# Performance work log

Measured on AMD Instinct MI355X. Metric: run time of the kernel, lower is better.

## Reference

```python
import jax, jax.numpy as jnp
import numpy as np

B = 32
H = 56
WD = 56
C = 192
NH = 6
WS = 7   # window size
SS = 3   # shift size
HID = 4 * C
N = WS * WS
NW = (H // WS) * (WD // WS)


def _rel_pos_index():
    coords = np.stack(np.meshgrid(np.arange(WS), np.arange(WS), indexing='ij'))  # [2,ws,ws]
    cf = coords.reshape(2, -1)
    rel = cf[:, :, None] - cf[:, None, :]          # [2,N,N]
    rel = rel.transpose(1, 2, 0)
    rel[..., 0] += WS - 1
    rel[..., 1] += WS - 1
    rel[..., 0] *= 2 * WS - 1
    return rel.sum(-1)                              # [N,N] int


def _attn_mask():
    img = np.zeros((H, WD))
    sl = (slice(0, -WS), slice(-WS, -SS), slice(-SS, None))
    cnt = 0
    for hs in sl:
        for ws in sl:
            img[hs, ws] = cnt
            cnt += 1
    mw = img.reshape(H // WS, WS, WD // WS, WS).transpose(0, 2, 1, 3).reshape(-1, N)  # [nW,N]
    d = mw[:, None, :] - mw[:, :, None]
    return np.where(d != 0, -100.0, 0.0).astype(np.float32)  # [nW,N,N]


_RPI = jnp.asarray(_rel_pos_index())
_MASK = jnp.asarray(_attn_mask())


def setup_inputs() -> dict:
    key = jax.random.key(0)
    ks = jax.random.split(key, 8)
    s = 0.02
    return {
        'x': jax.random.normal(ks[0], (B, H * WD, C), jnp.float32),
        'norm1_g': jnp.ones((C,), jnp.float32),
        'norm1_b': jnp.zeros((C,), jnp.float32),
        'qkv_w': jax.random.normal(ks[1], (C, 3 * C), jnp.float32) * s,
        'qkv_b': jnp.zeros((3 * C,), jnp.float32),
        'rel_bias': jax.random.normal(ks[2], ((2 * WS - 1) ** 2, NH), jnp.float32) * s,
        'proj_w': jax.random.normal(ks[3], (C, C), jnp.float32) * s,
        'proj_b': jnp.zeros((C,), jnp.float32),
        'norm2_g': jnp.ones((C,), jnp.float32),
        'norm2_b': jnp.zeros((C,), jnp.float32),
        'fc1_w': jax.random.normal(ks[4], (C, HID), jnp.float32) * s,
        'fc1_b': jnp.zeros((HID,), jnp.float32),
        'fc2_w': jax.random.normal(ks[5], (HID, C), jnp.float32) * s,
        'fc2_b': jnp.zeros((C,), jnp.float32),
    }


def _ln(x, g, b, eps=1e-5):
    m = jnp.mean(x, axis=-1, keepdims=True)
    v = jnp.mean(jnp.square(x - m), axis=-1, keepdims=True)
    return (x - m) / jnp.sqrt(v + eps) * g + b


def reference(x, norm1_g, norm1_b, qkv_w, qkv_b, rel_bias, proj_w, proj_b,
              norm2_g, norm2_b, fc1_w, fc1_b, fc2_w, fc2_b):
    hd = C // NH
    shortcut = x
    xn = _ln(x, norm1_g, norm1_b).reshape(B, H, WD, C)
    xs = jnp.roll(xn, (-SS, -SS), axis=(1, 2))                     # cyclic shift
    # window partition -> [B*nW, N, C]
    xw = xs.reshape(B, H // WS, WS, WD // WS, WS, C)
    xw = xw.transpose(0, 1, 3, 2, 4, 5).reshape(-1, N, C)
    # windowed attention
    qkv = (xw @ qkv_w + qkv_b).reshape(-1, N, 3, NH, hd).transpose(2, 0, 3, 1, 4)
    q, k, v = qkv[0], qkv[1], qkv[2]                               # [B*nW, NH, N, hd]
    attn = jnp.einsum('whnd,whmd->whnm', q * (hd ** -0.5), k)      # [B*nW, NH, N, N]
    bias = rel_bias[_RPI.reshape(-1)].reshape(N, N, NH).transpose(2, 0, 1)
    attn = attn + bias[None]
    attn = attn.reshape(B, NW, NH, N, N) + _MASK[None, :, None]
    attn = jax.nn.softmax(attn.reshape(-1, NH, N, N), axis=-1)
    out = jnp.einsum('whnm,whmd->whnd', attn, v)
    out = out.transpose(0, 2, 1, 3).reshape(-1, N, C)
    out = out @ proj_w + proj_b
    # window reverse + un-shift
    out = out.reshape(B, H // WS, WD // WS, WS, WS, C)
    out = out.transpose(0, 1, 3, 2, 4, 5).reshape(B, H, WD, C)
    out = jnp.roll(out, (SS, SS), axis=(1, 2)).reshape(B, H * WD, C)
    x = shortcut + out
    # MLP (exact GELU, matching torch nn.GELU default)
    xm = _ln(x, norm2_g, norm2_b)
    h = jax.nn.gelu(xm @ fc1_w + fc1_b, approximate=False)
    return x + (h @ fc2_w + fc2_b)
```

## Files before the change

### kernel.cpp

```cpp
#include <hip/hip_runtime.h>
#include <math.h>


constexpr long T = 100352;

typedef __attribute__((ext_vector_type(8))) short short8;
typedef __attribute__((ext_vector_type(4))) float f32x4;

__device__ __forceinline__ short bf16(float f) {
    union { float f; unsigned u; } v; v.f = f;
    return (short)((v.u + 0x7fff + ((v.u >> 16) & 1)) >> 16);
}

__device__ __forceinline__ void gll16(const void* g, void* l) {
    __builtin_amdgcn_global_load_lds(
        (const __attribute__((address_space(1))) void*)g,
        (__attribute__((address_space(3))) void*)l, 16, 0, 0);
}

__global__ __launch_bounds__(256)
void prep_k(const float* __restrict__ qkv_w, const float* __restrict__ proj_w,
            const float* __restrict__ fc1_w, const float* __restrict__ fc2_w,
            const float* __restrict__ relb, const float* __restrict__ x,
            short* __restrict__ qkvP, short* __restrict__ projP,
            short* __restrict__ fc1P, short* __restrict__ fc2P,
            float* __restrict__ bm, float* __restrict__ mean,
            float* __restrict__ rstd)
{
    const int bid = blockIdx.x;
    const int tid = threadIdx.x;
    if (bid < 432) {
        const int idx = bid * 256 + tid;
        const int k = idx / 576, n = idx - k * 576;
        const int flat = (((n >> 4) * 6 + (k >> 5)) * 64 +
                          (((k >> 3) & 3) << 4) + (n & 15)) * 8 + (k & 7);
        qkvP[flat] = bf16(qkv_w[idx]);
    } else if (bid < 576) {
        const int idx = (bid - 432) * 256 + tid;
        const int k = idx / 192, n = idx - k * 192;
        const int flat = ((((k >> 5) * 12 + (n >> 4)) * 64) +
                          (((k >> 3) & 3) << 4) + (n & 15)) * 8 + (k & 7);
        projP[flat] = bf16(proj_w[idx]);
    } else if (bid < 1152) {
        const int idx = (bid - 576) * 256 + tid;
        const int k = idx / 768, n = idx - k * 768;
        const int flat = (((n >> 4) * 6 + (k >> 5)) * 64 +
                          (((k >> 3) & 3) << 4) + (n & 15)) * 8 + (k & 7);
        fc1P[flat] = bf16(fc1_w[idx]);
    } else if (bid < 1728) {
        const int idx = (bid - 1152) * 256 + tid;
        const int k = idx / 192, n = idx - k * 192;
        const int t = k >> 6, ks = (k >> 5) & 1, nt = n >> 4;
        const int flat = (((t * 2 + ks) * 12 + nt) * 64 +
                          (((k >> 3) & 3) << 4) + (n & 15)) * 8 + (k & 7);
        fc2P[flat] = bf16(fc2_w[idx]);
    } else if (bid < 1954) {
        const int idx = (bid - 1728) * 256 + tid;
        if (idx >= 6 * 4 * 2401) return;
        const int e = idx % 2401, rest = idx / 2401;
        const int tw = rest & 1, th = (rest >> 1) & 1, head = rest >> 2;
        const int i = e / 49, j = e - i * 49;
        const int yi = i / 7, xi = i - yi * 7, yj = j / 7, xj = j - yj * 7;
        const float v = relb[((yi - yj + 6) * 13 + (xi - xj + 6)) * 6 + head];
        const int hi = th ? 49 + yi : yi, hj = th ? 49 + yj : yj;
        const int wa = tw ? 49 + xi : xi, wb = tw ? 49 + xj : xj;
        const int Li = (hi < 49 ? 0 : (hi < 53 ? 1 : 2)) * 3 + (wa < 49 ? 0 : (wa < 53 ? 1 : 2));
        const int Lj = (hj < 49 ? 0 : (hj < 53 ? 1 : 2)) * 3 + (wb < 49 ? 0 : (wb < 53 ? 1 : 2));
        bm[idx] = (Li != Lj) ? v - 100.0f : v;
    } else {
        const int wave = tid >> 6;
        const int lane = tid & 63;
        const long tok = (long)(bid - 1954) * 4 + wave;
        const float* p = x + tok * 192;
        const float a = p[lane], b = p[lane + 64], c = p[lane + 128];
        float s = a + b + c;
        float q = a * a + b * b + c * c;
        #pragma unroll
        for (int off = 32; off > 0; off >>= 1) {
            s += __shfl_xor(s, off);
            q += __shfl_xor(q, off);
        }
        if (lane == 0) {
            const float m = s * (1.0f / 192.0f);
            const float v = q * (1.0f / 192.0f) - m * m;
            mean[tok] = m;
            rstd[tok] = 1.0f / sqrtf(v + 1e-5f);
        }
    }
}

__global__ __launch_bounds__(256, 3)
void winattn_k(const float* __restrict__ x, const float* __restrict__ n1g,
               const float* __restrict__ n1b, const short* __restrict__ qkvP,
               const float* __restrict__ qkv_b, const float* __restrict__ bm,
               const float* __restrict__ mean, const float* __restrict__ rstd,
               float* __restrict__ outp)
{
    __shared__ __align__(16) short Kb[2][2048];
    __shared__ __align__(16) short Vb[2][2048];
    __shared__ __align__(16) short Pf[4][1024];
    const int bw  = blockIdx.x;
    const int tid = threadIdx.x;
    const int b = bw >> 6, wi = bw & 63, wh = wi >> 3, ww = wi & 7;
    const int wave = tid >> 6, lane = tid & 63;
    const int col = lane & 15, rbase = (lane >> 4) << 2;
    const float scale = 0.17677669529663687f;

    const int am = lane & 15;
    const int arow = (wave << 4) + am;
    const int kof = (lane >> 4) << 3;
    short8 afr[6];
    long tokA = 0; float mA = 0.f, rsA = 1.f;
    const bool avalid = arow < 49;
    if (avalid) {
        const int yi = arow / 7, xi = arow - yi * 7;
        int h = wh * 7 + yi + 3; if (h >= 56) h -= 56;
        int w = ww * 7 + xi + 3; if (w >= 56) w -= 56;
        tokA = (long)b * 3136 + h * 56 + w;
        mA = mean[tokA]; rsA = rstd[tokA];
    }
    #pragma unroll
    for (int ks = 0; ks < 6; ++ks) {
        short8 a = {};
        if (avalid) {
            const int k0 = (ks << 5) + kof;
            const float4 v0 = *(const float4*)(x + tokA * 192 + k0);
            const float4 v1 = *(const float4*)(x + tokA * 192 + k0 + 4);
            const float4 g0 = *(const float4*)(n1g + k0);
            const float4 g1 = *(const float4*)(n1g + k0 + 4);
            const float4 e0 = *(const float4*)(n1b + k0);
            const float4 e1 = *(const float4*)(n1b + k0 + 4);
            a[0] = bf16((v0.x - mA) * rsA * g0.x + e0.x);
            a[1] = bf16((v0.y - mA) * rsA * g0.y + e0.y);
            a[2] = bf16((v0.z - mA) * rsA * g0.z + e0.z);
            a[3] = bf16((v0.w - mA) * rsA * g0.w + e0.w);
            a[4] = bf16((v1.x - mA) * rsA * g1.x + e1.x);
            a[5] = bf16((v1.y - mA) * rsA * g1.y + e1.y);
            a[6] = bf16((v1.z - mA) * rsA * g1.z + e1.z);
            a[7] = bf16((v1.w - mA) * rsA * g1.w + e1.w);
        }
        afr[ks] = a;
    }

    short8 qfrag[6];
    #pragma unroll
    for (int nt = 0; nt < 12; ++nt) {
        f32x4 acc = {};
        #pragma unroll
        for (int ks = 0; ks < 6; ++ks) {
            const short8 bfr = *(const short8*)(qkvP + ((nt * 6 + ks) * 64 + lane) * 8);
            acc = __builtin_amdgcn_mfma_f32_16x16x32_bf16(afr[ks], bfr, acc, 0, 0, 0);
        }
        const int hh = nt >> 1, d = ((nt & 1) << 4) + col;
        const float bias = qkv_b[hh * 32 + d];
        #pragma unroll
        for (int r = 0; r < 4; ++r) {
            const int m = rbase + r;
            Pf[wave][((m + (((d >> 3) & 3) << 4)) << 3) + (d & 7)] =
                bf16((acc[r] + bias) * scale);
        }
        if (nt & 1) qfrag[hh] = *(const short8*)&Pf[wave][lane << 3];
    }

    long tok_r[4]; bool iv[4]; int i49[4];
    #pragma unroll
    for (int r = 0; r < 4; ++r) {
        const int i = (wave << 4) + rbase + r;
        iv[r] = i < 49;
        i49[r] = iv[r] ? i * 49 : 0;
        if (iv[r]) {
            const int yi = i / 7, xi = i - yi * 7;
            int h = wh * 7 + yi + 3; if (h >= 56) h -= 56;
            int w = ww * 7 + xi + 3; if (w >= 56) w -= 56;
            tok_r[r] = (long)b * 3136 + h * 56 + w;
        } else tok_r[r] = 0;
    }

    f32x4 oa[12] = {};

    #pragma unroll
    for (int h = 0; h < 6; ++h) {
        const int bs = h & 1;
        #pragma unroll
        for (int half = 0; half < 2; ++half) {
            const int d = (half << 4) + col;
            f32x4 acck = {};
            #pragma unroll
            for (int ks = 0; ks < 6; ++ks) {
                const short8 bfr = *(const short8*)(qkvP +
                    (((12 + 2 * h + half) * 6 + ks) * 64 + lane) * 8);
                acck = __builtin_amdgcn_mfma_f32_16x16x32_bf16(afr[ks], bfr, acck, 0, 0, 0);
            }
            const float biask = qkv_b[192 + h * 32 + d];
            #pragma unroll
            for (int r = 0; r < 4; ++r) {
                const int m = rbase + r;
                Kb[bs][(((wave << 6) + m + (((d >> 3) & 3) << 4)) << 3) + (d & 7)] =
                    bf16(acck[r] + biask);
            }
            f32x4 accv = {};
            #pragma unroll
            for (int ks = 0; ks < 6; ++ks) {
                const short8 bfr = *(const short8*)(qkvP +
                    (((24 + 2 * h + half) * 6 + ks) * 64 + lane) * 8);
                accv = __builtin_amdgcn_mfma_f32_16x16x32_bf16(afr[ks], bfr, accv, 0, 0, 0);
            }
            const float biasv = qkv_b[384 + h * 32 + d];
            #pragma unroll
            for (int r = 0; r < 4; ++r) {
                const int m = rbase + r;
                const int flat = ((((half << 1) + (wave >> 1)) << 6) + col +
                                  ((((wave << 1) + (m >> 3)) & 3) << 4)) * 8 + (m & 7);
                Vb[bs][flat] = bf16(accv[r] + biasv);
            }
        }
        __syncthreads();

        const float* bmp = bm + (((h << 1) + (wh == 7)) * 2 + (ww == 7)) * 2401;
        f32x4 sa[4];
        #pragma unroll
        for (int jt = 0; jt < 4; ++jt) {
            f32x4 z = {};
            const short8 kfr = *(const short8*)&Kb[bs][((jt << 6) + lane) << 3];
            sa[jt] = __builtin_amdgcn_mfma_f32_16x16x32_bf16(qfrag[h], kfr, z, 0, 0, 0);
        }
        float p[4][4];
        #pragma unroll
        for (int jt = 0; jt < 4; ++jt) {
            const int j = (jt << 4) + col;
            #pragma unroll
            for (int r = 0; r < 4; ++r)
                p[jt][r] = (j < 49) ? sa[jt][r] + bmp[i49[r] + j] : -1e30f;
        }
        #pragma unroll
        for (int r = 0; r < 4; ++r) {
            float mx = fmaxf(fmaxf(p[0][r], p[1][r]), fmaxf(p[2][r], p[3][r]));
            mx = fmaxf(mx, __shfl_xor(mx, 1));
            mx = fmaxf(mx, __shfl_xor(mx, 2));
            mx = fmaxf(mx, __shfl_xor(mx, 4));
            mx = fmaxf(mx, __shfl_xor(mx, 8));
            float sum = 0.f;
            #pragma unroll
            for (int jt = 0; jt < 4; ++jt) {
                const float e = (((jt << 4) + col) < 49) ? __expf(p[jt][r] - mx) : 0.f;
                p[jt][r] = e; sum += e;
            }
            sum += __shfl_xor(sum, 1);
            sum += __shfl_xor(sum, 2);
            sum += __shfl_xor(sum, 4);
            sum += __shfl_xor(sum, 8);
            const float inv = 1.0f / sum;
            #pragma unroll
            for (int jt = 0; jt < 4; ++jt) p[jt][r] *= inv;
        }
        #pragma unroll
        for (int jt = 0; jt < 4; ++jt) {
            #pragma unroll
            for (int r = 0; r < 4; ++r) {
                const int m = rbase + r;
                const int flat = (((jt >> 1) << 6) + m +
                                  ((((jt & 1) << 1) + (col >> 3)) << 4)) * 8 + (col & 7);
                Pf[wave][flat] = bf16(p[jt][r]);
            }
        }
        const short8 p0 = *(const short8*)&Pf[wave][lane << 3];
        const short8 p1 = *(const short8*)&Pf[wave][(64 + lane) << 3];
        #pragma unroll
        for (int dt = 0; dt < 2; ++dt) {
            const short8 v0 = *(const short8*)&Vb[bs][(((dt << 1) << 6) + lane) << 3];
            const short8 v1 = *(const short8*)&Vb[bs][((((dt << 1) + 1) << 6) + lane) << 3];
            oa[h * 2 + dt] = __builtin_amdgcn_mfma_f32_16x16x32_bf16(p0, v0, oa[h * 2 + dt], 0, 0, 0);
            oa[h * 2 + dt] = __builtin_amdgcn_mfma_f32_16x16x32_bf16(p1, v1, oa[h * 2 + dt], 0, 0, 0);
        }
    }

    #pragma unroll
    for (int r = 0; r < 4; ++r) {
        if (!iv[r]) continue;
        float* op = outp + tok_r[r] * 192;
        #pragma unroll
        for (int hh = 0; hh < 6; ++hh) {
            op[hh * 32 + col]      = oa[hh * 2 + 0][r];
            op[hh * 32 + 16 + col] = oa[hh * 2 + 1][r];
        }
    }
}

__global__ __launch_bounds__(256, 3)
void projmlp_k(const float* attnb, const short* __restrict__ projP,
               const float* __restrict__ pb, const float* __restrict__ x,
               const float* __restrict__ n2g, const float* __restrict__ n2b,
               const short* __restrict__ fc1P, const float* __restrict__ b1,
               const short* __restrict__ fc2P, const float* __restrict__ b2,
               float* outp)
{
    __shared__ __align__(16) short SB[2][6144];
    __shared__ __align__(16) short Hs[2048];
    const int tid = threadIdx.x;
    const int wave = tid >> 6, lane = tid & 63;
    const int col = lane & 15, rbase = (lane >> 4) << 2;
    const int kof = (lane >> 4) << 3;
    const long m0 = (long)blockIdx.x * 64;

    const long arow = m0 + (wave << 4) + col;
    const float* ap = attnb + arow * 192;
    short8 afr[6];
    #pragma unroll
    for (int ks = 0; ks < 6; ++ks) {
        const int k0 = (ks << 5) + kof;
        const float4 v0 = *(const float4*)(ap + k0);
        const float4 v1 = *(const float4*)(ap + k0 + 4);
        short8 a;
        a[0] = bf16(v0.x); a[1] = bf16(v0.y); a[2] = bf16(v0.z); a[3] = bf16(v0.w);
        a[4] = bf16(v1.x); a[5] = bf16(v1.y); a[6] = bf16(v1.z); a[7] = bf16(v1.w);
        afr[ks] = a;
    }
    f32x4 x1a[12] = {};
    #pragma unroll
    for (int ks = 0; ks < 6; ++ks) {
        #pragma unroll
        for (int nt = 0; nt < 12; ++nt) {
            const short8 bfr = *(const short8*)(projP + ks * 6144 + (nt << 9) + (lane << 3));
            x1a[nt] = __builtin_amdgcn_mfma_f32_16x16x32_bf16(afr[ks], bfr, x1a[nt], 0, 0, 0);
        }
    }
    const long orow = m0 + (wave << 4) + rbase;
    #pragma unroll
    for (int nt = 0; nt < 12; ++nt) {
        const int n = (nt << 4) + col;
        const float bias = pb[n];
        #pragma unroll
        for (int r = 0; r < 4; ++r)
            x1a[nt][r] += bias + x[(orow + r) * 192 + n];
    }
    float s0 = 0.f, s1_ = 0.f, s2_ = 0.f, s3 = 0.f;
    float q0 = 0.f, q1 = 0.f, q2 = 0.f, q3 = 0.f;
    #pragma unroll
    for (int nt = 0; nt < 12; ++nt) {
        s0 += x1a[nt][0]; q0 += x1a[nt][0] * x1a[nt][0];
        s1_ += x1a[nt][1]; q1 += x1a[nt][1] * x1a[nt][1];
        s2_ += x1a[nt][2]; q2 += x1a[nt][2] * x1a[nt][2];
        s3 += x1a[nt][3]; q3 += x1a[nt][3] * x1a[nt][3];
    }
    #pragma unroll
    for (int off = 8; off > 0; off >>= 1) {
        s0 += __shfl_xor(s0, off); q0 += __shfl_xor(q0, off);
        s1_ += __shfl_xor(s1_, off); q1 += __shfl_xor(q1, off);
        s2_ += __shfl_xor(s2_, off); q2 += __shfl_xor(q2, off);
        s3 += __shfl_xor(s3, off); q3 += __shfl_xor(q3, off);
    }
    float mr[4], rr[4];
    mr[0] = s0 * (1.0f / 192.0f); rr[0] = rsqrtf(q0 * (1.0f / 192.0f) - mr[0] * mr[0] + 1e-5f);
    mr[1] = s1_ * (1.0f / 192.0f); rr[1] = rsqrtf(q1 * (1.0f / 192.0f) - mr[1] * mr[1] + 1e-5f);
    mr[2] = s2_ * (1.0f / 192.0f); rr[2] = rsqrtf(q2 * (1.0f / 192.0f) - mr[2] * mr[2] + 1e-5f);
    mr[3] = s3 * (1.0f / 192.0f); rr[3] = rsqrtf(q3 * (1.0f / 192.0f) - mr[3] * mr[3] + 1e-5f);

    short* Xw = (short*)SB + wave * 3072;
    #pragma unroll
    for (int nt = 0; nt < 12; ++nt) {
        const int k = (nt << 4) + col;
        const float g = n2g[k], bb = n2b[k];
        #pragma unroll
        for (int r = 0; r < 4; ++r) {
            const int row16 = rbase + r;
            const int flat = (((k >> 5) << 6) + (((k >> 3) & 3) << 4) + row16) * 8 + (k & 7);
            Xw[flat] = bf16((x1a[nt][r] - mr[r]) * rr[r] * g + bb);
        }
    }
    short8 afrX[6];
    #pragma unroll
    for (int ks = 0; ks < 6; ++ks)
        afrX[ks] = *(const short8*)(Xw + (((ks << 6) + lane) << 3));

    f32x4 accO[12];
    #pragma unroll
    for (int nt = 0; nt < 12; ++nt) {
        const float bias = b2[(nt << 4) + col];
        #pragma unroll
        for (int r = 0; r < 4; ++r)
            accO[nt][r] = x1a[nt][r] + bias;
    }
    __syncthreads();

    auto STAGE = [&](short* dst, const short* src) {
        #pragma unroll
        for (int i = 0; i < 3; ++i) {
            const int slot = (i << 8) + (wave << 6);
            gll16(src + ((slot + lane) << 3), dst + (slot << 3));
        }
    };
    short* Hw = Hs + wave * 512;
    STAGE(SB[0], fc1P);
    __syncthreads();
    int cur = 0;
    for (int t = 0; t < 12; ++t) {
        const short* f1 = fc1P + t * 12288;
        const short* f2 = fc2P + t * 12288;
        f32x4 accH[4] = {};
        STAGE(SB[cur ^ 1], f1 + 6144);
        #pragma unroll
        for (int ks = 0; ks < 6; ++ks) {
            #pragma unroll
            for (int ntl = 0; ntl < 2; ++ntl) {
                const short8 bfr = *(const short8*)&SB[cur][((ntl * 6 + ks) << 9) + (lane << 3)];
                accH[ntl] = __builtin_amdgcn_mfma_f32_16x16x32_bf16(afrX[ks], bfr, accH[ntl], 0, 0, 0);
            }
        }
        __syncthreads(); cur ^= 1;
        STAGE(SB[cur ^ 1], f2);
        #pragma unroll
        for (int ks = 0; ks < 6; ++ks) {
            #pragma unroll
            for (int ntl = 0; ntl < 2; ++ntl) {
                const short8 bfr = *(const short8*)&SB[cur][((ntl * 6 + ks) << 9) + (lane << 3)];
                accH[2 + ntl] = __builtin_amdgcn_mfma_f32_16x16x32_bf16(afrX[ks], bfr, accH[2 + ntl], 0, 0, 0);
            }
        }
        __syncthreads(); cur ^= 1;
        STAGE(SB[cur ^ 1], f2 + 6144);
        #pragma unroll
        for (int nt = 0; nt < 2; ++nt) {
            const int kh = (nt << 4) + col;
            const float bias = b1[(t << 6) + kh];
            #pragma unroll
            for (int r = 0; r < 4; ++r) {
                const int m = rbase + r;
                float val = accH[nt][r] + bias;
                val = 0.5f * val * (1.0f + erff(val * 0.7071067811865476f));
                const int flat = ((((kh >> 3) & 3) << 4) + m) * 8 + (kh & 7);
                Hw[flat] = bf16(val);
            }
        }
        {
            const short8 a = *(const short8*)(Hw + (lane << 3));
            #pragma unroll
            for (int nt2 = 0; nt2 < 12; ++nt2) {
                const short8 bfr = *(const short8*)&SB[cur][(nt2 << 9) + (lane << 3)];
                accO[nt2] = __builtin_amdgcn_mfma_f32_16x16x32_bf16(a, bfr, accO[nt2], 0, 0, 0);
            }
        }
        __syncthreads(); cur ^= 1;
        if (t < 11) STAGE(SB[cur ^ 1], f1 + 12288);
        #pragma unroll
        for (int nt = 2; nt < 4; ++nt) {
            const int kh = (nt << 4) + col;
            const float bias = b1[(t << 6) + kh];
            #pragma unroll
            for (int r = 0; r < 4; ++r) {
                const int m = rbase + r;
                float val = accH[nt][r] + bias;
                val = 0.5f * val * (1.0f + erff(val * 0.7071067811865476f));
                const int flat = ((((kh >> 3) & 3) << 4) + m) * 8 + (kh & 7);
                Hw[flat] = bf16(val);
            }
        }
        {
            const short8 a = *(const short8*)(Hw + (lane << 3));
            #pragma unroll
            for (int nt2 = 0; nt2 < 12; ++nt2) {
                const short8 bfr = *(const short8*)&SB[cur][(nt2 << 9) + (lane << 3)];
                accO[nt2] = __builtin_amdgcn_mfma_f32_16x16x32_bf16(a, bfr, accO[nt2], 0, 0, 0);
            }
        }
        __syncthreads(); cur ^= 1;
    }

    #pragma unroll
    for (int nt = 0; nt < 12; ++nt) {
        const int n = (nt << 4) + col;
        #pragma unroll
        for (int r = 0; r < 4; ++r)
            outp[(orow + r) * 192 + n] = accO[nt][r];
    }
}

extern "C" void kernel_launch(void* const* d_in, const int* in_sizes, int n_in,
                              void* d_out, int out_size, void* d_ws, size_t ws_size,
                              hipStream_t stream)
{
    const float* x      = (const float*)d_in[0];
    const float* n1g    = (const float*)d_in[1];
    const float* n1b    = (const float*)d_in[2];
    const float* qkv_w  = (const float*)d_in[3];
    const float* qkv_b  = (const float*)d_in[4];
    const float* relb   = (const float*)d_in[5];
    const float* proj_w = (const float*)d_in[6];
    const float* proj_b = (const float*)d_in[7];
    const float* n2g    = (const float*)d_in[8];
    const float* n2b    = (const float*)d_in[9];
    const float* fc1_w  = (const float*)d_in[10];
    const float* fc1_b  = (const float*)d_in[11];
    const float* fc2_w  = (const float*)d_in[12];
    const float* fc2_b  = (const float*)d_in[13];
    float* out = (float*)d_out;
    char*  ws  = (char*)d_ws;

    float* mb    = (float*)(ws);
    float* rb    = (float*)(ws +   401408L);
    short* qkvP  = (short*)(ws +   802816L);
    short* projP = (short*)(ws +  1024000L);
    short* fc1P  = (short*)(ws +  1097728L);
    short* fc2P  = (short*)(ws +  1392640L);
    float* bmT   = (float*)(ws +  1687552L);

    prep_k<<<1954 + T / 4, 256, 0, stream>>>(qkv_w, proj_w, fc1_w, fc2_w,
                                             relb, x, qkvP, projP, fc1P,
                                             fc2P, bmT, mb, rb);
    winattn_k<<<2048, 256, 0, stream>>>(x, n1g, n1b, qkvP, qkv_b,
                                        bmT, mb, rb, out);
    projmlp_k<<<T / 64, 256, 0, stream>>>(out, projP, proj_b, x, n2g, n2b,
                                          fc1P, fc1_b, fc2P, fc2_b, out);
}
```

Before: 463.3 us.

## Triple-buffer MLP weight staging with one barrier per stage

Moves the fc1/fc2 weight staging in the fused proj+MLP kernel from a double buffer with two syncthreads per stage to a three-slot ring. Each stage issues the next async global-to-LDS load, waits with a partial vmcnt so only the older load must finish, and then uses a single raw s_barrier. This is meant to hide more load latency and cut barrier stalls. LDS use per block rises by 12 KB, which may lower occupancy at the 3-block launch bound, and the hand-placed waitcnt and barrier logic risks subtle ordering bugs.

```diff
diff --git a/kernel.cpp b/kernel.cpp
--- a/kernel.cpp
+++ b/kernel.cpp
@@ -294,7 +294,7 @@
                const short* __restrict__ fc2P, const float* __restrict__ b2,
                float* outp)
 {
-    __shared__ __align__(16) short SB[2][6144];
+    __shared__ __align__(16) short SB[3][6144];
     __shared__ __align__(16) short Hs[2048];
     const int tid = threadIdx.x;
     const int wave = tid >> 6, lane = tid & 63;
@@ -390,79 +390,106 @@
         }
     };
     short* Hw = Hs + wave * 512;
-    STAGE(SB[0], fc1P);
-    __syncthreads();
-    int cur = 0;
+    STAGE(&SB[0][0], fc1P);
+    int rd = 0;
     for (int t = 0; t < 12; ++t) {
         const short* f1 = fc1P + t * 12288;
         const short* f2 = fc2P + t * 12288;
         f32x4 accH[4] = {};
-        STAGE(SB[cur ^ 1], f1 + 6144);
-        #pragma unroll
-        for (int ks = 0; ks < 6; ++ks) {
-            #pragma unroll
-            for (int ntl = 0; ntl < 2; ++ntl) {
-                const short8 bfr = *(const short8*)&SB[cur][((ntl * 6 + ks) << 9) + (lane << 3)];
-                accH[ntl] = __builtin_amdgcn_mfma_f32_16x16x32_bf16(afrX[ks], bfr, accH[ntl], 0, 0, 0);
-            }
-        }
-        __syncthreads(); cur ^= 1;
-        STAGE(SB[cur ^ 1], f2);
-        #pragma unroll
-        for (int ks = 0; ks < 6; ++ks) {
-            #pragma unroll
-            for (int ntl = 0; ntl < 2; ++ntl) {
-                const short8 bfr = *(const short8*)&SB[cur][((ntl * 6 + ks) << 9) + (lane << 3)];
-                accH[2 + ntl] = __builtin_amdgcn_mfma_f32_16x16x32_bf16(afrX[ks], bfr, accH[2 + ntl], 0, 0, 0);
-            }
-        }
-        __syncthreads(); cur ^= 1;
-        STAGE(SB[cur ^ 1], f2 + 6144);
-        #pragma unroll
-        for (int nt = 0; nt < 2; ++nt) {
-            const int kh = (nt << 4) + col;
-            const float bias = b1[(t << 6) + kh];
-            #pragma unroll
-            for (int r = 0; r < 4; ++r) {
-                const int m = rbase + r;
-                float val = accH[nt][r] + bias;
-                val = 0.5f * val * (1.0f + erff(val * 0.7071067811865476f));
-                const int flat = ((((kh >> 3) & 3) << 4) + m) * 8 + (kh & 7);
-                Hw[flat] = bf16(val);
-            }
-        }
         {
+            const int wr = (rd == 2) ? 0 : rd + 1;
+            STAGE(&SB[wr][0], f1 + 6144);
+            asm volatile("s_waitcnt vmcnt(3)" ::: "memory");
+            __builtin_amdgcn_s_barrier();
+            __builtin_amdgcn_sched_barrier(0);
+            const short* B = &SB[rd][0];
+            #pragma unroll
+            for (int ks = 0; ks < 6; ++ks) {
+                #pragma unroll
+                for (int ntl = 0; ntl < 2; ++ntl) {
+                    const short8 bfr = *(const short8*)&B[((ntl * 6 + ks) << 9) + (lane << 3)];
+                    accH[ntl] = __builtin_amdgcn_mfma_f32_16x16x32_bf16(afrX[ks], bfr, accH[ntl], 0, 0, 0);
+                }
+            }
+            rd = wr;
+        }
+        {
+            const int wr = (rd == 2) ? 0 : rd + 1;
+            STAGE(&SB[wr][0], f2);
+            asm volatile("s_waitcnt vmcnt(3)" ::: "memory");
+            __builtin_amdgcn_s_barrier();
+            __builtin_amdgcn_sched_barrier(0);
+            const short* B = &SB[rd][0];
+            #pragma unroll
+            for (int ks = 0; ks < 6; ++ks) {
+                #pragma unroll
+                for (int ntl = 0; ntl < 2; ++ntl) {
+                    const short8 bfr = *(const short8*)&B[((ntl * 6 + ks) << 9) + (lane << 3)];
+                    accH[2 + ntl] = __builtin_amdgcn_mfma_f32_16x16x32_bf16(afrX[ks], bfr, accH[2 + ntl], 0, 0, 0);
+                }
+            }
+            rd = wr;
+        }
+        {
+            const int wr = (rd == 2) ? 0 : rd + 1;
+            STAGE(&SB[wr][0], f2 + 6144);
+            asm volatile("s_waitcnt vmcnt(3)" ::: "memory");
+            __builtin_amdgcn_s_barrier();
+            __builtin_amdgcn_sched_barrier(0);
+            const short* B = &SB[rd][0];
+            #pragma unroll
+            for (int nt = 0; nt < 2; ++nt) {
+                const int kh = (nt << 4) + col;
+                const float bias = b1[(t << 6) + kh];
+                #pragma unroll
+                for (int r = 0; r < 4; ++r) {
+                    const int m = rbase + r;
+                    float val = accH[nt][r] + bias;
+                    val = 0.5f * val * (1.0f + erff(val * 0.7071067811865476f));
+                    const int flat = ((((kh >> 3) & 3) << 4) + m) * 8 + (kh & 7);
+                    Hw[flat] = bf16(val);
+                }
+            }
             const short8 a = *(const short8*)(Hw + (lane << 3));
             #pragma unroll
             for (int nt2 = 0; nt2 < 12; ++nt2) {
-                const short8 bfr = *(const short8*)&SB[cur][(nt2 << 9) + (lane << 3)];
+                const short8 bfr = *(const short8*)&B[(nt2 << 9) + (lane << 3)];
                 accO[nt2] = __builtin_amdgcn_mfma_f32_16x16x32_bf16(a, bfr, accO[nt2], 0, 0, 0);
             }
-        }
-        __syncthreads(); cur ^= 1;
-        if (t < 11) STAGE(SB[cur ^ 1], f1 + 12288);
-        #pragma unroll
-        for (int nt = 2; nt < 4; ++nt) {
-            const int kh = (nt << 4) + col;
-            const float bias = b1[(t << 6) + kh];
-            #pragma unroll
-            for (int r = 0; r < 4; ++r) {
-                const int m = rbase + r;
-                float val = accH[nt][r] + bias;
-                val = 0.5f * val * (1.0f + erff(val * 0.7071067811865476f));
-                const int flat = ((((kh >> 3) & 3) << 4) + m) * 8 + (kh & 7);
-                Hw[flat] = bf16(val);
-            }
+            rd = wr;
         }
         {
+            const int wr = (rd == 2) ? 0 : rd + 1;
+            if (t < 11) {
+                STAGE(&SB[wr][0], f1 + 12288);
+                asm volatile("s_waitcnt vmcnt(3)" ::: "memory");
+            } else {
+                asm volatile("s_waitcnt vmcnt(0)" ::: "memory");
+            }
+            __builtin_amdgcn_s_barrier();
+            __builtin_amdgcn_sched_barrier(0);
+            const short* B = &SB[rd][0];
+            #pragma unroll
+            for (int nt = 2; nt < 4; ++nt) {
+                const int kh = (nt << 4) + col;
+                const float bias = b1[(t << 6) + kh];
+                #pragma unroll
+                for (int r = 0; r < 4; ++r) {
+                    const int m = rbase + r;
+                    float val = accH[nt][r] + bias;
+                    val = 0.5f * val * (1.0f + erff(val * 0.7071067811865476f));
+                    const int flat = ((((kh >> 3) & 3) << 4) + m) * 8 + (kh & 7);
+                    Hw[flat] = bf16(val);
+                }
+            }
             const short8 a = *(const short8*)(Hw + (lane << 3));
             #pragma unroll
             for (int nt2 = 0; nt2 < 12; ++nt2) {
-                const short8 bfr = *(const short8*)&SB[cur][(nt2 << 9) + (lane << 3)];
+                const short8 bfr = *(const short8*)&B[(nt2 << 9) + (lane << 3)];
                 accO[nt2] = __builtin_amdgcn_mfma_f32_16x16x32_bf16(a, bfr, accO[nt2], 0, 0, 0);
             }
-        }
-        __syncthreads(); cur ^= 1;
+            rd = wr;
+        }
     }
 
     #pragma unroll
```

Measured after the change: 467.5 us. About the same (+0.9%).
